# Kernel tuning notes

Hardware: AMD Instinct MI355X
Metric: run time of the kernel (lower is better)

Reference implementation:

```python
import jax, jax.numpy as jnp
import numpy as np

B, NI, NO = 4, 256, 256          # batch, num_in, num_out
DIN, DQ, DH, DOUT = 256, 256, 256, 256


def setup_inputs() -> dict:
    key = jax.random.key(0)
    ks = jax.random.split(key, 6)
    def w(k, shape, fan_in):
        return jax.random.normal(k, shape, jnp.float32) / np.sqrt(fan_in).astype(np.float32)
    return {
        "x": jax.random.normal(ks[0], (B, NI, DIN), jnp.float32),
        "query": jax.random.normal(ks[1], (B, NO, DQ), jnp.float32),
        # pre_cond_mlp: Linear(DIN -> DH)
        "W_pre": w(ks[2], (DIN, DH), DIN), "b_pre": jnp.zeros((DH,), jnp.float32),
        # cond_embed: Linear(DQ -> DH)
        "W_emb": w(ks[3], (DQ, DH), DQ), "b_emb": jnp.zeros((DH,), jnp.float32),
        # post_cond_mlp: Linear(2*DH -> DH) + GELU + Linear(DH -> DOUT)
        "W1": w(ks[4], (2 * DH, DH), 2 * DH), "b1": jnp.zeros((DH,), jnp.float32),
        "W2": w(ks[5], (DH, DOUT), DH), "b2": jnp.zeros((DOUT,), jnp.float32),
    }


def reference(x, query, W_pre, b_pre, W_emb, b_emb, W1, b1, W2, b2):
    # pre_cond_mlp(x): [B, NI, DH]
    xp = x @ W_pre + b_pre
    # cond_embed(query): [B, NO, DH]
    c = query @ W_emb + b_emb
    # Original torch code: repeat xp over NO, c over NI, concat -> [B,NI,NO,2*DH],
    # then Linear(2*DH->DH). Algebraically identical (and far cheaper) to split W1
    # and broadcast-add the two projections:
    W1x, W1c = W1[:DH], W1[DH:]          # [DH, DH] each
    h = (xp @ W1x)[:, :, None, :] + (c @ W1c)[:, None, :, :] + b1  # [B, NI, NO, DH]
    h = jax.nn.gelu(h, approximate=False)  # torch nn.GELU default = exact erf
    return h @ W2 + b2                     # [B, NI, NO, DOUT]
```

## Files before the change

### kernel.cpp

```cpp
#include <hip/hip_runtime.h>
#include <hip/hip_bf16.h>
#include <cstdint>
#include <cstddef>


typedef __bf16  bf16x8 __attribute__((ext_vector_type(8)));
typedef float   f32x16 __attribute__((ext_vector_type(16)));

__device__ __forceinline__ float fast_gelu(float x) {
    const float x2 = x * x;
    const float m  = __builtin_fmaf(x2, -0.1029433f, -2.3022072f);
    const float e  = __builtin_amdgcn_exp2f(x * m);
    return x * __builtin_amdgcn_rcpf(1.0f + e);
}

__global__ __launch_bounds__(256) void prep_kernel(
    const float* __restrict__ x, const float* __restrict__ query,
    const float* __restrict__ W_pre, const float* __restrict__ b_pre,
    const float* __restrict__ W_emb, const float* __restrict__ b_emb,
    const float* __restrict__ W1, const float* __restrict__ b1,
    const float* __restrict__ W2,
    float* __restrict__ u, float* __restrict__ v,
    unsigned short* __restrict__ w2f)
{
    const int b = blockIdx.x;
    const int t = threadIdx.x;

    if (b >= 512) {
        const int n0 = (b - 512) * 4;
        const float4 wv = *reinterpret_cast<const float4*>(W2 + (size_t)t * 256 + n0);
        const float vals[4] = {wv.x, wv.y, wv.z, wv.w};
        const int g = t >> 3, e = t & 7;
#pragma unroll
        for (int j = 0; j < 4; ++j) {
            const __bf16 bv = (__bf16)vals[j];
            w2f[((size_t)(g * 256 + n0 + j)) * 8 + e] =
                __builtin_bit_cast(unsigned short, bv);
        }
        return;
    }

    const bool isq = (b >= 256);
    const float* __restrict__ A   = isq ? query : x;
    const float* __restrict__ Wa  = isq ? W_emb : W_pre;
    const float* __restrict__ ba  = isq ? b_emb : b_pre;
    const float* __restrict__ W1p = isq ? (W1 + 256 * 256) : W1;
    float* __restrict__ outp      = isq ? v : u;
    const int r0 = (isq ? (b - 256) : b) * 4;

    __shared__ float as[4][256];
    __shared__ float xs[4][256];

#pragma unroll
    for (int r = 0; r < 4; ++r)
        as[r][t] = A[(size_t)(r0 + r) * 256 + t];
    __syncthreads();

    float acc[4] = {0.f, 0.f, 0.f, 0.f};
    {
        float wcur[8];
#pragma unroll
        for (int q = 0; q < 8; ++q) wcur[q] = Wa[(size_t)q * 256 + t];
        for (int k0 = 0; k0 < 248; k0 += 8) {
            float wnxt[8];
#pragma unroll
            for (int q = 0; q < 8; ++q)
                wnxt[q] = Wa[(size_t)(k0 + 8 + q) * 256 + t];
#pragma unroll
            for (int q = 0; q < 8; ++q)
#pragma unroll
                for (int r = 0; r < 4; ++r)
                    acc[r] = __builtin_fmaf(as[r][k0 + q], wcur[q], acc[r]);
#pragma unroll
            for (int q = 0; q < 8; ++q) wcur[q] = wnxt[q];
        }
#pragma unroll
        for (int q = 0; q < 8; ++q)
#pragma unroll
            for (int r = 0; r < 4; ++r)
                acc[r] = __builtin_fmaf(as[r][248 + q], wcur[q], acc[r]);
    }
    const float bav = ba[t];
#pragma unroll
    for (int r = 0; r < 4; ++r) xs[r][t] = acc[r] + bav;
    __syncthreads();

    float acc2[4] = {0.f, 0.f, 0.f, 0.f};
    {
        float wcur[8];
#pragma unroll
        for (int q = 0; q < 8; ++q) wcur[q] = W1p[(size_t)q * 256 + t];
        for (int k0 = 0; k0 < 248; k0 += 8) {
            float wnxt[8];
#pragma unroll
            for (int q = 0; q < 8; ++q)
                wnxt[q] = W1p[(size_t)(k0 + 8 + q) * 256 + t];
#pragma unroll
            for (int q = 0; q < 8; ++q)
#pragma unroll
                for (int r = 0; r < 4; ++r)
                    acc2[r] = __builtin_fmaf(xs[r][k0 + q], wcur[q], acc2[r]);
#pragma unroll
            for (int q = 0; q < 8; ++q) wcur[q] = wnxt[q];
        }
#pragma unroll
        for (int q = 0; q < 8; ++q)
#pragma unroll
            for (int r = 0; r < 4; ++r)
                acc2[r] = __builtin_fmaf(xs[r][248 + q], wcur[q], acc2[r]);
    }
    const float b1v = isq ? 0.f : b1[t];
#pragma unroll
    for (int r = 0; r < 4; ++r)
        outp[(size_t)(r0 + r) * 256 + t] = acc2[r] + b1v;
}

__global__ __launch_bounds__(256, 3) void fused_kernel(
    const float* __restrict__ U, const float* __restrict__ V,
    const unsigned short* __restrict__ W2F, const float* __restrict__ b2,
    float* __restrict__ out)
{
    __shared__ uint4 hlds[1024];
    __shared__ uint4 blds[2][1024];
    unsigned int* const h32 = reinterpret_cast<unsigned int*>(hlds);

    const int t    = threadIdx.x;
    const int lane = t & 63;
    const int w    = t >> 6;
    const int l31  = lane & 31;
    const int hi   = lane >> 5;

    const int bid  = blockIdx.x;
    const int tile = bid >> 1;
    const int jh   = bid & 1;
    const int bb   = tile >> 8;

    const float* __restrict__ urow  = U + (size_t)tile * 256;
    const float* __restrict__ vbase = V + ((size_t)(bb * 256 + jh * 128)) * 256;

    const int d = l31;

    auto stage_b = [&](int cg, int buf) {
#pragma unroll
        for (int it = 0; it < 4; ++it) {
            const int idx = it * 256 + t;
            const int g   = idx >> 5;
            const int c   = idx & 31;
            __builtin_amdgcn_global_load_lds(
                (const __attribute__((address_space(1))) unsigned int*)
                    (W2F + ((size_t)(g * 256 + cg * 32 + c)) * 8),
                (__attribute__((address_space(3))) unsigned int*)
                    (&blds[buf][idx]),
                16, 0, 0);
        }
    };

    stage_b(0, 0);

    bf16x8 af[16];
    const int arow = w * 32 + l31;
#pragma unroll
    for (int c = 0; c < 4; ++c) {
        const int kk = c * 64;
        const float2 u2 = *reinterpret_cast<const float2*>(urow + kk + 2 * d);
        float2 vv[16];
#pragma unroll
        for (int p = 0; p < 16; ++p) {
            const int row = w * 32 + p * 2 + hi;
            vv[p] = *reinterpret_cast<const float2*>(
                vbase + (size_t)row * 256 + kk + 2 * d);
        }
#pragma unroll
        for (int p = 0; p < 16; ++p) {
            const int row = w * 32 + p * 2 + hi;
            union { unsigned int u32; __bf16 h[2]; } pk;
            pk.h[0] = (__bf16)fast_gelu(u2.x + vv[p].x);
            pk.h[1] = (__bf16)fast_gelu(u2.y + vv[p].y);
            h32[row * 32 + (((d >> 2) ^ (row & 7)) << 2) + (d & 3)] = pk.u32;
        }
#pragma unroll
        for (int s = 0; s < 4; ++s) {
            const int gl = 2 * s + hi;
            af[c * 4 + s] = __builtin_bit_cast(
                bf16x8, hlds[arow * 8 + (gl ^ (arow & 7))]);
        }
    }

    float bvv[8];
#pragma unroll
    for (int cg = 0; cg < 8; ++cg) bvv[cg] = b2[cg * 32 + l31];

    const size_t obase = ((size_t)tile << 16) + (size_t)(jh * 128 + w * 32) * 256;

#pragma unroll
    for (int cg = 0; cg < 8; ++cg) {
        if (cg < 7) stage_b(cg + 1, (cg + 1) & 1);

        f32x16 acc = (f32x16)0.f;
#pragma unroll
        for (int S = 0; S < 16; ++S) {
            const bf16x8 bf_ = __builtin_bit_cast(
                bf16x8, blds[cg & 1][(2 * S + hi) * 32 + l31]);
            acc = __builtin_amdgcn_mfma_f32_32x32x16_bf16(af[S], bf_, acc, 0, 0, 0);
        }

        __syncthreads();

        const int col = cg * 32 + l31;
#pragma unroll
        for (int rr = 0; rr < 16; ++rr) {
            const int row = 4 * hi + (rr & 3) + 8 * (rr >> 2);
            out[obase + (size_t)row * 256 + col] = acc[rr] + bvv[cg];
        }
    }
}

extern "C" void kernel_launch(void* const* d_in, const int* in_sizes, int n_in,
                              void* d_out, int out_size, void* d_ws, size_t ws_size,
                              hipStream_t stream)
{
    const float* x     = (const float*)d_in[0];
    const float* query = (const float*)d_in[1];
    const float* W_pre = (const float*)d_in[2];
    const float* b_pre = (const float*)d_in[3];
    const float* W_emb = (const float*)d_in[4];
    const float* b_emb = (const float*)d_in[5];
    const float* W1    = (const float*)d_in[6];
    const float* b1    = (const float*)d_in[7];
    const float* W2    = (const float*)d_in[8];
    const float* b2    = (const float*)d_in[9];
    float* out = (float*)d_out;

    char* ws = (char*)d_ws;
    float* u            = (float*)(ws);
    float* v            = (float*)(ws + (1 << 20));
    unsigned short* w2f = (unsigned short*)(ws + 2 * (1 << 20));

    prep_kernel<<<576, 256, 0, stream>>>(x, query, W_pre, b_pre, W_emb, b_emb,
                                         W1, b1, W2, u, v, w2f);
    fused_kernel<<<2048, 256, 0, stream>>>(u, v, w2f, b2, out);
}
```

Measured before the change: 92.50 us.

## Use single-wave blocks and read W2 fragments directly from global memory

The fused kernel now runs one 64-thread wave per block over a 32-row slab, launching 8192 blocks instead of 2048 four-wave blocks. The double-buffered LDS staging of W2 tiles and the per-step __syncthreads are removed, and each wave loads its MFMA B fragments straight from global memory. The aim is to drop barriers, cut LDS use and raise occupancy and scheduling flexibility. In exchange, every wave re-reads W2 from L2/L1 with no sharing through LDS, which raises memory traffic and exposes load latency ahead of each MFMA.

```diff
diff --git a/kernel.cpp b/kernel.cpp
--- a/kernel.cpp
+++ b/kernel.cpp
@@ -115,50 +115,30 @@
         outp[(size_t)(r0 + r) * 256 + t] = acc2[r] + b1v;
 }
 
-__global__ __launch_bounds__(256, 3) void fused_kernel(
+__global__ __launch_bounds__(64, 3) void fused_kernel(
     const float* __restrict__ U, const float* __restrict__ V,
     const unsigned short* __restrict__ W2F, const float* __restrict__ b2,
     float* __restrict__ out)
 {
-    __shared__ uint4 hlds[1024];
-    __shared__ uint4 blds[2][1024];
+    __shared__ uint4 hlds[256];
     unsigned int* const h32 = reinterpret_cast<unsigned int*>(hlds);
 
-    const int t    = threadIdx.x;
-    const int lane = t & 63;
-    const int w    = t >> 6;
-    const int l31  = lane & 31;
-    const int hi   = lane >> 5;
+    const int t   = threadIdx.x;
+    const int l31 = t & 31;
+    const int hi  = t >> 5;
 
     const int bid  = blockIdx.x;
-    const int tile = bid >> 1;
-    const int jh   = bid & 1;
+    const int tile = bid >> 3;
+    const int slab = bid & 7;
     const int bb   = tile >> 8;
 
     const float* __restrict__ urow  = U + (size_t)tile * 256;
-    const float* __restrict__ vbase = V + ((size_t)(bb * 256 + jh * 128)) * 256;
-
-    const int d = l31;
-
-    auto stage_b = [&](int cg, int buf) {
-#pragma unroll
-        for (int it = 0; it < 4; ++it) {
-            const int idx = it * 256 + t;
-            const int g   = idx >> 5;
-            const int c   = idx & 31;
-            __builtin_amdgcn_global_load_lds(
-                (const __attribute__((address_space(1))) unsigned int*)
-                    (W2F + ((size_t)(g * 256 + cg * 32 + c)) * 8),
-                (__attribute__((address_space(3))) unsigned int*)
-                    (&blds[buf][idx]),
-                16, 0, 0);
-        }
-    };
-
-    stage_b(0, 0);
+    const float* __restrict__ vbase = V + ((size_t)(bb * 256 + slab * 32)) * 256;
+
+    const int d    = l31;
+    const int arow = l31;
 
     bf16x8 af[16];
-    const int arow = w * 32 + l31;
 #pragma unroll
     for (int c = 0; c < 4; ++c) {
         const int kk = c * 64;
@@ -166,13 +146,13 @@
         float2 vv[16];
 #pragma unroll
         for (int p = 0; p < 16; ++p) {
-            const int row = w * 32 + p * 2 + hi;
+            const int row = p * 2 + hi;
             vv[p] = *reinterpret_cast<const float2*>(
                 vbase + (size_t)row * 256 + kk + 2 * d);
         }
 #pragma unroll
         for (int p = 0; p < 16; ++p) {
-            const int row = w * 32 + p * 2 + hi;
+            const int row = p * 2 + hi;
             union { unsigned int u32; __bf16 h[2]; } pk;
             pk.h[0] = (__bf16)fast_gelu(u2.x + vv[p].x);
             pk.h[1] = (__bf16)fast_gelu(u2.y + vv[p].y);
@@ -190,21 +170,18 @@
 #pragma unroll
     for (int cg = 0; cg < 8; ++cg) bvv[cg] = b2[cg * 32 + l31];
 
-    const size_t obase = ((size_t)tile << 16) + (size_t)(jh * 128 + w * 32) * 256;
+    const size_t obase = ((size_t)tile << 16) + (size_t)(slab * 32) * 256;
 
 #pragma unroll
     for (int cg = 0; cg < 8; ++cg) {
-        if (cg < 7) stage_b(cg + 1, (cg + 1) & 1);
-
         f32x16 acc = (f32x16)0.f;
 #pragma unroll
         for (int S = 0; S < 16; ++S) {
-            const bf16x8 bf_ = __builtin_bit_cast(
-                bf16x8, blds[cg & 1][(2 * S + hi) * 32 + l31]);
+            const uint4 braw = *reinterpret_cast<const uint4*>(
+                W2F + ((size_t)((2 * S + hi) * 256 + cg * 32 + l31)) * 8);
+            const bf16x8 bf_ = __builtin_bit_cast(bf16x8, braw);
             acc = __builtin_amdgcn_mfma_f32_32x32x16_bf16(af[S], bf_, acc, 0, 0, 0);
         }
-
-        __syncthreads();
 
         const int col = cg * 32 + l31;
 #pragma unroll
@@ -238,5 +215,5 @@
 
     prep_kernel<<<576, 256, 0, stream>>>(x, query, W_pre, b_pre, W_emb, b_emb,
                                          W1, b1, W2, u, v, w2f);
-    fused_kernel<<<2048, 256, 0, stream>>>(u, v, w2f, b2, out);
-}
+    fused_kernel<<<8192, 64, 0, stream>>>(u, v, w2f, b2, out);
+}
```

New measurement: 185.7 us. +100.8%, slower.

## Store V transposed to build GELU MFMA fragments directly in registers

Applied to the files above, without the earlier changes.

The prep kernel now writes the query projection transposed (vt[b][d][j]). The fused kernel can then load each lane's eight k-contiguous V values directly and build its bf16 A fragments in registers. This drops the 16KB LDS staging buffer for h and its swizzled write/read round trip, which lowers LDS usage and may raise occupancy. In exchange, the prep kernel does strided, poorly coalesced transposed stores, and the fused kernel issues eight scalar strided V loads per fragment. The barrier placement is also reshuffled: one barrier before the MFMA loop and one at the end of each iteration.

```diff
diff --git a/kernel.cpp b/kernel.cpp
--- a/kernel.cpp
+++ b/kernel.cpp
@@ -20,7 +20,7 @@
     const float* __restrict__ W_emb, const float* __restrict__ b_emb,
     const float* __restrict__ W1, const float* __restrict__ b1,
     const float* __restrict__ W2,
-    float* __restrict__ u, float* __restrict__ v,
+    float* __restrict__ u, float* __restrict__ vt,
     unsigned short* __restrict__ w2f)
 {
     const int b = blockIdx.x;
@@ -45,7 +45,6 @@
     const float* __restrict__ Wa  = isq ? W_emb : W_pre;
     const float* __restrict__ ba  = isq ? b_emb : b_pre;
     const float* __restrict__ W1p = isq ? (W1 + 256 * 256) : W1;
-    float* __restrict__ outp      = isq ? v : u;
     const int r0 = (isq ? (b - 256) : b) * 4;
 
     __shared__ float as[4][256];
@@ -109,20 +108,27 @@
             for (int r = 0; r < 4; ++r)
                 acc2[r] = __builtin_fmaf(xs[r][248 + q], wcur[q], acc2[r]);
     }
-    const float b1v = isq ? 0.f : b1[t];
-#pragma unroll
-    for (int r = 0; r < 4; ++r)
-        outp[(size_t)(r0 + r) * 256 + t] = acc2[r] + b1v;
+
+    if (!isq) {
+        const float b1v = b1[t];
+#pragma unroll
+        for (int r = 0; r < 4; ++r)
+            u[(size_t)(r0 + r) * 256 + t] = acc2[r] + b1v;
+    } else {
+        const int bb = r0 >> 8;
+        const int jb = r0 & 255;
+#pragma unroll
+        for (int r = 0; r < 4; ++r)
+            vt[((size_t)(bb * 256 + t)) * 256 + (jb + r)] = acc2[r];
+    }
 }
 
 __global__ __launch_bounds__(256, 3) void fused_kernel(
-    const float* __restrict__ U, const float* __restrict__ V,
+    const float* __restrict__ U, const float* __restrict__ VT,
     const unsigned short* __restrict__ W2F, const float* __restrict__ b2,
     float* __restrict__ out)
 {
-    __shared__ uint4 hlds[1024];
     __shared__ uint4 blds[2][1024];
-    unsigned int* const h32 = reinterpret_cast<unsigned int*>(hlds);
 
     const int t    = threadIdx.x;
     const int lane = t & 63;
@@ -135,10 +141,10 @@
     const int jh   = bid & 1;
     const int bb   = tile >> 8;
 
-    const float* __restrict__ urow  = U + (size_t)tile * 256;
-    const float* __restrict__ vbase = V + ((size_t)(bb * 256 + jh * 128)) * 256;
-
-    const int d = l31;
+    const float* __restrict__ urow = U + (size_t)tile * 256;
+    const int jloc = jh * 128 + w * 32 + l31;
+    const float* __restrict__ vtcol =
+        VT + ((size_t)(bb * 256)) * 256 + jloc;
 
     auto stage_b = [&](int cg, int buf) {
 #pragma unroll
@@ -158,32 +164,26 @@
     stage_b(0, 0);
 
     bf16x8 af[16];
-    const int arow = w * 32 + l31;
-#pragma unroll
-    for (int c = 0; c < 4; ++c) {
-        const int kk = c * 64;
-        const float2 u2 = *reinterpret_cast<const float2*>(urow + kk + 2 * d);
-        float2 vv[16];
-#pragma unroll
-        for (int p = 0; p < 16; ++p) {
-            const int row = w * 32 + p * 2 + hi;
-            vv[p] = *reinterpret_cast<const float2*>(
-                vbase + (size_t)row * 256 + kk + 2 * d);
-        }
-#pragma unroll
-        for (int p = 0; p < 16; ++p) {
-            const int row = w * 32 + p * 2 + hi;
-            union { unsigned int u32; __bf16 h[2]; } pk;
-            pk.h[0] = (__bf16)fast_gelu(u2.x + vv[p].x);
-            pk.h[1] = (__bf16)fast_gelu(u2.y + vv[p].y);
-            h32[row * 32 + (((d >> 2) ^ (row & 7)) << 2) + (d & 3)] = pk.u32;
-        }
-#pragma unroll
-        for (int s = 0; s < 4; ++s) {
-            const int gl = 2 * s + hi;
-            af[c * 4 + s] = __builtin_bit_cast(
-                bf16x8, hlds[arow * 8 + (gl ^ (arow & 7))]);
-        }
+#pragma unroll
+    for (int S = 0; S < 16; ++S) {
+        const int kb = S * 16 + hi * 8;
+        const float4 ua = *reinterpret_cast<const float4*>(urow + kb);
+        const float4 ub = *reinterpret_cast<const float4*>(urow + kb + 4);
+        float vtv[8];
+#pragma unroll
+        for (int e = 0; e < 8; ++e)
+            vtv[e] = vtcol[(size_t)(kb + e) * 256];
+
+        bf16x8 a;
+        a[0] = (__bf16)fast_gelu(ua.x + vtv[0]);
+        a[1] = (__bf16)fast_gelu(ua.y + vtv[1]);
+        a[2] = (__bf16)fast_gelu(ua.z + vtv[2]);
+        a[3] = (__bf16)fast_gelu(ua.w + vtv[3]);
+        a[4] = (__bf16)fast_gelu(ub.x + vtv[4]);
+        a[5] = (__bf16)fast_gelu(ub.y + vtv[5]);
+        a[6] = (__bf16)fast_gelu(ub.z + vtv[6]);
+        a[7] = (__bf16)fast_gelu(ub.w + vtv[7]);
+        af[S] = a;
     }
 
     float bvv[8];
@@ -191,6 +191,8 @@
     for (int cg = 0; cg < 8; ++cg) bvv[cg] = b2[cg * 32 + l31];
 
     const size_t obase = ((size_t)tile << 16) + (size_t)(jh * 128 + w * 32) * 256;
+
+    __syncthreads();
 
 #pragma unroll
     for (int cg = 0; cg < 8; ++cg) {
@@ -204,14 +206,13 @@
             acc = __builtin_amdgcn_mfma_f32_32x32x16_bf16(af[S], bf_, acc, 0, 0, 0);
         }
 
-        __syncthreads();
-
         const int col = cg * 32 + l31;
 #pragma unroll
         for (int rr = 0; rr < 16; ++rr) {
             const int row = 4 * hi + (rr & 3) + 8 * (rr >> 2);
             out[obase + (size_t)row * 256 + col] = acc[rr] + bvv[cg];
         }
+        __syncthreads();
     }
 }
 
@@ -233,10 +234,10 @@
 
     char* ws = (char*)d_ws;
     float* u            = (float*)(ws);
-    float* v            = (float*)(ws + (1 << 20));
+    float* vt           = (float*)(ws + (1 << 20));
     unsigned short* w2f = (unsigned short*)(ws + 2 * (1 << 20));
 
     prep_kernel<<<576, 256, 0, stream>>>(x, query, W_pre, b_pre, W_emb, b_emb,
-                                         W1, b1, W2, u, v, w2f);
-    fused_kernel<<<2048, 256, 0, stream>>>(u, v, w2f, b2, out);
-}
+                                         W1, b1, W2, u, vt, w2f);
+    fused_kernel<<<2048, 256, 0, stream>>>(u, vt, w2f, b2, out);
+}
```

After: 106.7 us. +15.3%, slower.
